# Optimization experiments

Hardware: AMD Instinct MI355X
Metric: run time of the kernel (lower is better)

Reference implementation:

```python
import jax, jax.numpy as jnp
import numpy as np

B, L, H = 32, 256, 128
VOCAB = 10


def _conv1d(h, w, b, dilation):
    # h: [B, C_in, T], w: [C_out, C_in, K] (torch OIH layout), 'same' padding = dilation for K=3
    y = jax.lax.conv_general_dilated(
        h, w, window_strides=(1,), padding=[(dilation, dilation)],
        rhs_dilation=(dilation,), dimension_numbers=("NCH", "OIH", "NCH"))
    return y + b[None, :, None]


def setup_inputs() -> dict:
    key = jax.random.key(0)
    ks = jax.random.split(key, 8)
    x = jax.random.randint(ks[0], (B, L), 0, VOCAB)
    emb_w = jax.random.normal(ks[1], (VOCAB, H), dtype=jnp.float32)
    red_w = jax.random.normal(ks[2], (H, 2 * H, 1), dtype=jnp.float32) * 0.05
    red_b = jax.random.normal(ks[3], (H,), dtype=jnp.float32) * 0.05
    conv_w = jax.random.normal(ks[4], (H, H, 3), dtype=jnp.float32) * 0.002
    conv_b = jax.random.normal(ks[5], (H,), dtype=jnp.float32) * 0.01
    out_w = jax.random.normal(ks[6], (VOCAB, H, 1), dtype=jnp.float32) * 0.1
    out_b = jax.random.normal(ks[7], (VOCAB,), dtype=jnp.float32) * 0.1
    return {"x": x, "emb_w": emb_w, "red_w": red_w, "red_b": red_b,
            "conv_w": conv_w, "conv_b": conv_b, "out_w": out_w, "out_b": out_b}


def reference(x, emb_w, red_w, red_b, conv_w, conv_b, out_w, out_b):
    digits = L // 2
    x_emb = emb_w[x].transpose(0, 2, 1)                 # [B, H, L]
    cat = jnp.concatenate([x_emb[:, :, :digits], x_emb[:, :, digits:]], axis=1)  # [B, 2H, digits]
    # reducer: 1x1 conv == pointwise matmul
    h = jax.nn.relu(jnp.einsum('oc,bct->bot', red_w[:, :, 0], cat) + red_b[None, :, None])
    h = jnp.pad(h, ((0, 0), (0, 0), (0, 1)))            # [B, H, digits+1]
    loop_count = digits + 1 + 2                          # = digits + 3
    # first 8 iterations: dilation 1 (i<4) then 2 (i<8); remainder uses dilation 4
    for i in range(min(8, loop_count)):
        d = 1 if i < 4 else 2
        h = jax.nn.relu(_conv1d(h, conv_w, conv_b, d)) + h
    def step(hc, _):
        hc = jax.nn.relu(_conv1d(hc, conv_w, conv_b, 4)) + hc
        return hc, None
    h, _ = jax.lax.scan(step, h, None, length=max(0, loop_count - 8))
    out = jnp.einsum('oc,bct->bot', out_w[:, :, 0], h) + out_b[None, :, None]  # [B, 10, digits+1]
    return out.transpose(0, 2, 1)                        # [B, digits+1, 10]
```

## Files before the change

kernel.cpp:

```cpp
#include <hip/hip_runtime.h>

typedef __attribute__((ext_vector_type(8))) short short8;
typedef __attribute__((ext_vector_type(4))) float f32x4;
typedef __attribute__((ext_vector_type(16))) float f32x16;

#define I2ROWS 40
#define I2STRIDE (I2ROWS * 128)
#define P1ROWS 72
#define P1STRIDE (P1ROWS * 128)
#define GWOFF 1056768

template<int N> struct IC { static constexpr int v = N; };

static __device__ __forceinline__ unsigned packbf(float hi, float lo) {
    return __builtin_amdgcn_perm(__float_as_uint(hi) + 0x8000u,
                                 __float_as_uint(lo) + 0x8000u, 0x07060302u);
}
static __device__ __forceinline__ unsigned short one_bf(float f) {
    return (unsigned short)((__float_as_uint(f) + 0x8000u) >> 16);
}
static __device__ __forceinline__ float bflo(unsigned u) { return __uint_as_float(u << 16); }
static __device__ __forceinline__ float bfhi(unsigned u) { return __uint_as_float(u & 0xffff0000u); }

static __device__ __forceinline__ int swzB(int row, int c) {
    return row * 128 + (c ^ ((row & 15) << 3));
}
static __device__ __forceinline__ int swzH(int t, int o) {
    return (t * 128 + o) ^ ((t & 15) << 1);
}

__global__ __launch_bounds__(256, 1)
void vgt_tab(const float* __restrict__ emb_w, const float* __restrict__ red_w,
             float* __restrict__ tab)
{
    int i = blockIdx.x * 256 + threadIdx.x;
    if (i >= 2560) return;
    int o = i / 20, col = i % 20, v = (col < 10) ? col : (col - 10);
    const float4* rw = (const float4*)(red_w + o * 256 + ((col < 10) ? 0 : 128));
    const float4* ew = (const float4*)(emb_w + v * 128);
    float s = 0.f;
#pragma unroll 8
    for (int c2 = 0; c2 < 32; ++c2) {
        float4 a = rw[c2], e = ew[c2];
        s += a.x * e.x + a.y * e.y + a.z * e.z + a.w * e.w;
    }
    tab[i] = s;
}

__global__ __launch_bounds__(256, 1)
void vgt_phase1(const int* __restrict__ x,
                const float* __restrict__ red_b,
                const float* __restrict__ conv_w,
                const float* __restrict__ conv_b,
                const float* __restrict__ tab,
                unsigned short* __restrict__ gw16)
{
    __shared__ short imgC[2 * P1STRIDE];
    __shared__ float hrFC[64 * 128];
    __shared__ float tabS[2560];
    __shared__ float cbS[128];
    __shared__ float rbS[128];
    __shared__ int   xbS[256];

    const int bid = blockIdx.x, b = bid >> 2, c = bid & 3;
    const int os = c * 33, oe = (os + 33 > 129) ? 129 : (os + 33), ws = os - 14;
    const int tid = threadIdx.x, lane = tid & 63;
    const int wm = tid >> 6, obase = wm * 32;
    const int l31 = lane & 31, lhi = lane >> 5;

    for (int i = tid; i < P1STRIDE; i += 256) ((int*)imgC)[i] = 0;
    for (int i = tid; i < 2560; i += 256) tabS[i] = tab[i];
    xbS[tid] = x[b * 256 + tid];
    if (tid < 128) { cbS[tid] = conv_b[tid]; rbS[tid] = red_b[tid]; }

    short8 aw[24];
#pragma unroll
    for (int s = 0; s < 24; ++s) {
        int kk = s >> 3, cb = s & 7;
        int o = obase + l31, c0 = cb * 16 + lhi * 8;
        short8 v;
#pragma unroll
        for (int j = 0; j < 8; ++j)
            v[j] = (short)one_bf(conv_w[(o * 128 + c0 + j) * 3 + kk]);
        aw[s] = v;
    }
    __syncthreads();

    for (int i = tid; i < 68 * 64; i += 256) {
        int rr = i >> 6, o2 = (i & 63) * 2, t = ws - 2 + rr;
        float v0 = 0.f, v1 = 0.f;
        if (t >= 0 && t < 128) {
            int x1 = xbS[t], x2 = xbS[t + 128];
            v0 = tabS[o2 * 20 + x1] + tabS[o2 * 20 + 10 + x2] + rbS[o2];
            v0 = v0 > 0.f ? v0 : 0.f;
            v1 = tabS[(o2 + 1) * 20 + x1] + tabS[(o2 + 1) * 20 + 10 + x2] + rbS[o2 + 1];
            v1 = v1 > 0.f ? v1 : 0.f;
            *(unsigned*)&imgC[swzB(rr, o2)] = packbf(v1, v0);
        }
        int rm = rr - 2;
        if (rm >= 0 && rm < 64) *(float2*)&hrFC[swzH(rm, o2)] = make_float2(v0, v1);
    }
    __syncthreads();

    int cur = 0;
    auto tileC = [&](auto DDC, int n, const short* src, short* dst) {
        constexpr int DD = decltype(DDC)::v;
        f32x16 a0, a1, a2;
#pragma unroll
        for (int g = 0; g < 4; ++g) {
            float4 bv = *(const float4*)&cbS[obase + 8 * g + 4 * lhi];
            a0[4*g+0] = bv.x; a0[4*g+1] = bv.y; a0[4*g+2] = bv.z; a0[4*g+3] = bv.w;
            a1[4*g+0] = 0.f; a1[4*g+1] = 0.f; a1[4*g+2] = 0.f; a1[4*g+3] = 0.f;
            a2[4*g+0] = 0.f; a2[4*g+1] = 0.f; a2[4*g+2] = 0.f; a2[4*g+3] = 0.f;
        }
        const int rb0 = n * 32 + l31 + 2 - DD;
#define TAPC(KK, ACC) { const int row = rb0 + KK * DD; \
    _Pragma("unroll") for (int cb = 0; cb < 8; ++cb) { \
        short8 bf = *(const short8*)&src[swzB(row, cb * 16 + lhi * 8)]; \
        ACC = __builtin_amdgcn_mfma_f32_32x32x16_bf16(aw[KK * 8 + cb], bf, ACC, 0, 0, 0); } }
        TAPC(0, a0) TAPC(1, a1) TAPC(2, a2)
#undef TAPC
        const int t = ws + n * 32 + l31;
        if (t >= 0 && t <= 128) {
            const int rm = n * 32 + l31;
#pragma unroll
            for (int g = 0; g < 4; ++g) {
                const int o4 = obase + 8 * g + 4 * lhi;
                const int h0 = swzH(rm, o4), h1 = swzH(rm, o4 + 2);
                float2 ha = *(const float2*)&hrFC[h0];
                float2 hb = *(const float2*)&hrFC[h1];
                ha.x += fmaxf(a0[4*g+0] + a1[4*g+0] + a2[4*g+0], 0.f);
                ha.y += fmaxf(a0[4*g+1] + a1[4*g+1] + a2[4*g+1], 0.f);
                hb.x += fmaxf(a0[4*g+2] + a1[4*g+2] + a2[4*g+2], 0.f);
                hb.y += fmaxf(a0[4*g+3] + a1[4*g+3] + a2[4*g+3], 0.f);
                *(float2*)&hrFC[h0] = ha;
                *(float2*)&hrFC[h1] = hb;
                *(uint2*)&dst[swzB(rm + 2, o4)] =
                    make_uint2(packbf(ha.y, ha.x), packbf(hb.y, hb.x));
            }
        }
    };
    auto step1 = [&](auto DDC) {
        const short* src = imgC + cur * P1STRIDE;
        short*       dst = imgC + (cur ^ 1) * P1STRIDE;
        tileC(DDC, 0, src, dst);
        tileC(DDC, 1, src, dst);
        __syncthreads();
        cur ^= 1;
    };
    for (int i = 0; i < 4; ++i) step1(IC<1>{});
    for (int i = 0; i < 4; ++i) step1(IC<2>{});

    for (int i = tid; i < (oe - os) * 128; i += 256) {
        int t = os + (i >> 7), o = i & 127;
        gw16[b * 16512 + t * 128 + o] = one_bf(hrFC[swzH(t - ws, o)]);
    }
}

__global__ __launch_bounds__(512, 1)
void vgt_phase2(const float* __restrict__ conv_w,
                const float* __restrict__ conv_b,
                const float* __restrict__ out_w,
                const float* __restrict__ out_b,
                const unsigned short* __restrict__ gw16,
                float* __restrict__ out)
{
    __shared__ short    img2[2 * I2STRIDE];
    __shared__ float    hrF2[33 * 128];
    __shared__ unsigned owP[10][64];
    __shared__ float    cbS[128];
    __shared__ float    obS[16];

    const int bid = blockIdx.x, b = bid >> 2, r = bid & 3;
    const int tid = threadIdx.x, lane = tid & 63;
    const int wv = tid >> 6;
    const int obase = wv * 16;
    const int l15 = lane & 15, g4 = lane >> 4;

    for (int i = tid; i < I2STRIDE; i += 512) ((int*)img2)[i] = 0;
    if (tid < 128) cbS[tid] = conv_b[tid];
    if (tid < 16)  obS[tid] = (tid < 10) ? out_b[tid] : 0.f;
    for (int i = tid; i < 640; i += 512) {
        int v = i >> 6, j = i & 63;
        owP[v][j] = packbf(out_w[v * 128 + 2 * j + 1], out_w[v * 128 + 2 * j]);
    }

    short8 aw[12];
#pragma unroll
    for (int s = 0; s < 12; ++s) {
        int kk = s >> 2, kb = s & 3;
        int o = obase + l15, c0 = kb * 32 + g4 * 8;
        short8 v;
#pragma unroll
        for (int j = 0; j < 8; ++j)
            v[j] = (short)one_bf(conv_w[(o * 128 + c0 + j) * 3 + kk]);
        aw[s] = v;
    }

    const unsigned short* gb = gw16 + b * 16512;
    float hm[2][4], hA[4];
#pragma unroll
    for (int tt = 0; tt < 2; ++tt) {
        int tp = tt * 16 + l15;
#pragma unroll
        for (int q = 0; q < 4; ++q)
            hm[tt][q] = bflo((unsigned)gb[(4 * tp + r) * 128 + obase + g4 * 4 + q]);
    }
#pragma unroll
    for (int q = 0; q < 4; ++q)
        hA[q] = (r == 0) ? bflo((unsigned)gb[16384 + obase + g4 * 4 + q]) : 0.f;

    int aM[12], aA[8], aWr, aWA;
#pragma unroll
    for (int s = 0; s < 12; ++s)
        aM[s] = 2 * swzB(l15 + (s >> 2), (s & 3) * 32 + g4 * 8);
#pragma unroll
    for (int s = 0; s < 8; ++s)
        aA[s] = 2 * swzB(32 + (s >> 2), (s & 3) * 32 + g4 * 8);
    aWr = 2 * swzB(l15 + 1, obase + g4 * 4);
    aWA = 2 * swzB(33, obase + g4 * 4);

    __syncthreads();

    float bias4[4];
#pragma unroll
    for (int q = 0; q < 4; ++q) bias4[q] = cbS[obase + g4 * 4 + q];

    for (int i = tid; i < 33 * 64; i += 512) {
        int tp = i >> 6, o2 = (i & 63) * 2;
        if (tp < 32) {
            unsigned u0 = gb[(4 * tp + r) * 128 + o2], u1 = gb[(4 * tp + r) * 128 + o2 + 1];
            *(unsigned*)&img2[swzB(tp + 1, o2)] = (u1 << 16) | u0;
        } else if (r == 0) {
            unsigned u0 = gb[16384 + o2], u1 = gb[16384 + o2 + 1];
            *(unsigned*)&img2[swzB(33, o2)] = (u1 << 16) | u0;
        }
    }
    __syncthreads();

    char* const ibase = (char*)img2;

    auto stepF = [&](auto SO_, auto DO_) {
        constexpr int SO = decltype(SO_)::v;
        constexpr int DO = decltype(DO_)::v;
        f32x4 c00, c01, c10, c11;
#pragma unroll
        for (int q = 0; q < 4; ++q) {
            c00[q] = bias4[q]; c10[q] = bias4[q];
            c01[q] = 0.f; c11[q] = 0.f;
        }
#pragma unroll
        for (int s = 0; s < 8; ++s) {
            short8 b0 = *(const short8*)(ibase + aM[s] + SO);
            short8 b1 = *(const short8*)(ibase + aM[s] + 4096 + SO);
            c00 = __builtin_amdgcn_mfma_f32_16x16x32_bf16(aw[s], b0, c00, 0, 0, 0);
            c10 = __builtin_amdgcn_mfma_f32_16x16x32_bf16(aw[s], b1, c10, 0, 0, 0);
        }
#pragma unroll
        for (int s = 8; s < 12; ++s) {
            short8 b0 = *(const short8*)(ibase + aM[s] + SO);
            short8 b1 = *(const short8*)(ibase + aM[s] + 4096 + SO);
            c01 = __builtin_amdgcn_mfma_f32_16x16x32_bf16(aw[s], b0, c01, 0, 0, 0);
            c11 = __builtin_amdgcn_mfma_f32_16x16x32_bf16(aw[s], b1, c11, 0, 0, 0);
        }
        {
#pragma unroll
            for (int q = 0; q < 4; ++q) hm[0][q] += fmaxf(c00[q] + c01[q], 0.f);
            *(uint2*)(ibase + aWr + DO) =
                make_uint2(packbf(hm[0][1], hm[0][0]), packbf(hm[0][3], hm[0][2]));
#pragma unroll
            for (int q = 0; q < 4; ++q) hm[1][q] += fmaxf(c10[q] + c11[q], 0.f);
            *(uint2*)(ibase + aWr + 4096 + DO) =
                make_uint2(packbf(hm[1][1], hm[1][0]), packbf(hm[1][3], hm[1][2]));
        }
        if (r == 0) {
            f32x4 d0, d1;
#pragma unroll
            for (int q = 0; q < 4; ++q) { d0[q] = bias4[q]; d1[q] = 0.f; }
#pragma unroll
            for (int s = 0; s < 4; ++s) {
                short8 bf = *(const short8*)(ibase + aA[s] + SO);
                d0 = __builtin_amdgcn_mfma_f32_16x16x32_bf16(aw[s], bf, d0, 0, 0, 0);
            }
#pragma unroll
            for (int s = 4; s < 8; ++s) {
                short8 bf = *(const short8*)(ibase + aA[s] + SO);
                d1 = __builtin_amdgcn_mfma_f32_16x16x32_bf16(aw[s], bf, d1, 0, 0, 0);
            }
#pragma unroll
            for (int q = 0; q < 4; ++q) hA[q] += fmaxf(d0[q] + d1[q], 0.f);
            if (l15 == 0)
                *(uint2*)(ibase + aWA + DO) =
                    make_uint2(packbf(hA[1], hA[0]), packbf(hA[3], hA[2]));
        }
        __syncthreads();
    };

    for (int i2 = 0; i2 < 61; ++i2) {
        stepF(IC<0>{}, IC<10240>{});
        stepF(IC<10240>{}, IC<0>{});
    }
    stepF(IC<0>{}, IC<10240>{});

#pragma unroll
    for (int tt = 0; tt < 2; ++tt)
        *(float4*)&hrF2[(tt * 16 + l15) * 128 + obase + g4 * 4] =
            make_float4(hm[tt][0], hm[tt][1], hm[tt][2], hm[tt][3]);
    if (r == 0 && l15 == 0)
        *(float4*)&hrF2[32 * 128 + obase + g4 * 4] =
            make_float4(hA[0], hA[1], hA[2], hA[3]);
    __syncthreads();

    const int g4h = tid & 3;
    const int tt = tid >> 2;
    const int TR = (r == 0) ? 33 : 32;
    if (tt < TR) {
        float hq[32];
#pragma unroll
        for (int j = 0; j < 8; ++j) {
            float4 v = *(const float4*)&hrF2[tt * 128 + 32 * g4h + 4 * j];
            hq[4*j+0] = v.x; hq[4*j+1] = v.y; hq[4*j+2] = v.z; hq[4*j+3] = v.w;
        }
#pragma unroll
        for (int v = 0; v < 10; ++v) {
            float s = 0.f;
#pragma unroll
            for (int i = 0; i < 16; ++i) {
                unsigned w = owP[v][16 * g4h + i];
                s += hq[2*i] * bflo(w) + hq[2*i+1] * bfhi(w);
            }
            s += __shfl_xor(s, 1);
            s += __shfl_xor(s, 2);
            if (g4h == 0) out[(b * 129 + 4 * tt + r) * 10 + v] = s + obS[v];
        }
    }
}

extern "C" void kernel_launch(void* const* d_in, const int* in_sizes, int n_in,
                              void* d_out, int out_size, void* d_ws, size_t ws_size,
                              hipStream_t stream) {
    const int*   x      = (const int*)d_in[0];
    const float* emb_w  = (const float*)d_in[1];
    const float* red_w  = (const float*)d_in[2];
    const float* red_b  = (const float*)d_in[3];
    const float* conv_w = (const float*)d_in[4];
    const float* conv_b = (const float*)d_in[5];
    const float* out_w  = (const float*)d_in[6];
    const float* out_b  = (const float*)d_in[7];
    (void)in_sizes; (void)n_in; (void)ws_size; (void)out_size;
    unsigned short* gw16 = (unsigned short*)d_ws;
    float* tab = (float*)((char*)d_ws + GWOFF);
    vgt_tab<<<10, 256, 0, stream>>>(emb_w, red_w, tab);
    vgt_phase1<<<128, 256, 0, stream>>>(x, red_b, conv_w, conv_b, tab, gw16);
    vgt_phase2<<<128, 512, 0, stream>>>(conv_w, conv_b, out_w, out_b, gw16, (float*)d_out);
}
```

Measured before the change: 170.4 us.

## Split conv reduction across wave pairs with LDS partial-sum exchange

Changes the phase-2 work split so each wave computes a 32-output by 64-channel tile, with two wave roles that each cover half the input channels. Partial sums go through a new LDS buffer and are combined by the role-0 waves, which own the residual state. Each B-operand load from the image now feeds four MFMAs instead of two, cutting LDS reads per MFMA. In exchange every step gains an extra barrier plus LDS write/read traffic for the partials, and the serial 123-step recurrence is latency bound.

```diff
diff --git a/kernel.cpp b/kernel.cpp
--- a/kernel.cpp
+++ b/kernel.cpp
@@ -166,6 +166,7 @@
                 float* __restrict__ out)
 {
     __shared__ short    img2[2 * I2STRIDE];
+    __shared__ float    pbuf[6 * 1024];
     __shared__ float    hrF2[33 * 128];
     __shared__ unsigned owP[10][64];
     __shared__ float    cbS[128];
@@ -174,7 +175,10 @@
     const int bid = blockIdx.x, b = bid >> 2, r = bid & 3;
     const int tid = threadIdx.x, lane = tid & 63;
     const int wv = tid >> 6;
-    const int obase = wv * 16;
+    const int pr = wv & 3;
+    const int role = wv >> 2;
+    const int obase = pr * 32;
+    const int chbase = role * 64;
     const int l15 = lane & 15, g4 = lane >> 4;
 
     for (int i = tid; i < I2STRIDE; i += 512) ((int*)img2)[i] = 0;
@@ -187,44 +191,63 @@
 
     short8 aw[12];
 #pragma unroll
-    for (int s = 0; s < 12; ++s) {
-        int kk = s >> 2, kb = s & 3;
-        int o = obase + l15, c0 = kb * 32 + g4 * 8;
-        short8 v;
-#pragma unroll
-        for (int j = 0; j < 8; ++j)
-            v[j] = (short)one_bf(conv_w[(o * 128 + c0 + j) * 3 + kk]);
-        aw[s] = v;
+    for (int s = 0; s < 6; ++s) {
+        int kk = s >> 1, cb = s & 1;
+        int c0 = chbase + cb * 32 + g4 * 8;
+#pragma unroll
+        for (int mt = 0; mt < 2; ++mt) {
+            int o = obase + mt * 16 + l15;
+            short8 v;
+#pragma unroll
+            for (int j = 0; j < 8; ++j)
+                v[j] = (short)one_bf(conv_w[(o * 128 + c0 + j) * 3 + kk]);
+            aw[s * 2 + mt] = v;
+        }
     }
 
     const unsigned short* gb = gw16 + b * 16512;
-    float hm[2][4], hA[4];
-#pragma unroll
-    for (int tt = 0; tt < 2; ++tt) {
-        int tp = tt * 16 + l15;
-#pragma unroll
-        for (int q = 0; q < 4; ++q)
-            hm[tt][q] = bflo((unsigned)gb[(4 * tp + r) * 128 + obase + g4 * 4 + q]);
-    }
-#pragma unroll
-    for (int q = 0; q < 4; ++q)
-        hA[q] = (r == 0) ? bflo((unsigned)gb[16384 + obase + g4 * 4 + q]) : 0.f;
-
-    int aM[12], aA[8], aWr, aWA;
-#pragma unroll
-    for (int s = 0; s < 12; ++s)
-        aM[s] = 2 * swzB(l15 + (s >> 2), (s & 3) * 32 + g4 * 8);
-#pragma unroll
-    for (int s = 0; s < 8; ++s)
-        aA[s] = 2 * swzB(32 + (s >> 2), (s & 3) * 32 + g4 * 8);
-    aWr = 2 * swzB(l15 + 1, obase + g4 * 4);
-    aWA = 2 * swzB(33, obase + g4 * 4);
+
+    float hm00[4], hm01[4], hm10[4], hm11[4];
+    float hA0[4], hA1[4];
+    if (role == 0) {
+#pragma unroll
+        for (int q = 0; q < 4; ++q) {
+            hm00[q] = bflo((unsigned)gb[(4 * l15 + r) * 128 + obase + g4 * 4 + q]);
+            hm01[q] = bflo((unsigned)gb[(4 * l15 + r) * 128 + obase + 16 + g4 * 4 + q]);
+            hm10[q] = bflo((unsigned)gb[(4 * (16 + l15) + r) * 128 + obase + g4 * 4 + q]);
+            hm11[q] = bflo((unsigned)gb[(4 * (16 + l15) + r) * 128 + obase + 16 + g4 * 4 + q]);
+        }
+    } else {
+#pragma unroll
+        for (int q = 0; q < 4; ++q) {
+            hA0[q] = (r == 0) ? bflo((unsigned)gb[16384 + obase + g4 * 4 + q]) : 0.f;
+            hA1[q] = (r == 0) ? bflo((unsigned)gb[16384 + obase + 16 + g4 * 4 + q]) : 0.f;
+        }
+    }
+
+    int aM[6], aA[4], aW00, aW01, aW10, aW11, aWA0, aWA1;
+#pragma unroll
+    for (int s = 0; s < 6; ++s)
+        aM[s] = 2 * swzB(l15 + (s >> 1), chbase + (s & 1) * 32 + g4 * 8);
+#pragma unroll
+    for (int s = 0; s < 4; ++s)
+        aA[s] = 2 * swzB(32 + (s >> 1), chbase + (s & 1) * 32 + g4 * 8);
+    aW00 = 2 * swzB(l15 + 1, obase + g4 * 4);
+    aW01 = 2 * swzB(l15 + 1, obase + 16 + g4 * 4);
+    aW10 = 2 * swzB(16 + l15 + 1, obase + g4 * 4);
+    aW11 = 2 * swzB(16 + l15 + 1, obase + 16 + g4 * 4);
+    aWA0 = 2 * swzB(33, obase + g4 * 4);
+    aWA1 = 2 * swzB(33, obase + 16 + g4 * 4);
+    const int pAddr = pr * 1024 + lane * 16;
 
     __syncthreads();
 
-    float bias4[4];
-#pragma unroll
-    for (int q = 0; q < 4; ++q) bias4[q] = cbS[obase + g4 * 4 + q];
+    float bb[8];
+#pragma unroll
+    for (int q = 0; q < 4; ++q) {
+        bb[q]     = cbS[obase + g4 * 4 + q];
+        bb[4 + q] = cbS[obase + 16 + g4 * 4 + q];
+    }
 
     for (int i = tid; i < 33 * 64; i += 512) {
         int tp = i >> 6, o2 = (i & 63) * 2;
@@ -239,59 +262,87 @@
     __syncthreads();
 
     char* const ibase = (char*)img2;
+    char* const pB = (char*)pbuf;
 
     auto stepF = [&](auto SO_, auto DO_) {
         constexpr int SO = decltype(SO_)::v;
         constexpr int DO = decltype(DO_)::v;
-        f32x4 c00, c01, c10, c11;
-#pragma unroll
-        for (int q = 0; q < 4; ++q) {
-            c00[q] = bias4[q]; c10[q] = bias4[q];
-            c01[q] = 0.f; c11[q] = 0.f;
-        }
-#pragma unroll
-        for (int s = 0; s < 8; ++s) {
+        f32x4 a00, a01, a10, a11;
+#pragma unroll
+        for (int q = 0; q < 4; ++q) { a00[q] = 0.f; a01[q] = 0.f; a10[q] = 0.f; a11[q] = 0.f; }
+#pragma unroll
+        for (int s = 0; s < 6; ++s) {
             short8 b0 = *(const short8*)(ibase + aM[s] + SO);
             short8 b1 = *(const short8*)(ibase + aM[s] + 4096 + SO);
-            c00 = __builtin_amdgcn_mfma_f32_16x16x32_bf16(aw[s], b0, c00, 0, 0, 0);
-            c10 = __builtin_amdgcn_mfma_f32_16x16x32_bf16(aw[s], b1, c10, 0, 0, 0);
-        }
-#pragma unroll
-        for (int s = 8; s < 12; ++s) {
-            short8 b0 = *(const short8*)(ibase + aM[s] + SO);
-            short8 b1 = *(const short8*)(ibase + aM[s] + 4096 + SO);
-            c01 = __builtin_amdgcn_mfma_f32_16x16x32_bf16(aw[s], b0, c01, 0, 0, 0);
-            c11 = __builtin_amdgcn_mfma_f32_16x16x32_bf16(aw[s], b1, c11, 0, 0, 0);
-        }
-        {
-#pragma unroll
-            for (int q = 0; q < 4; ++q) hm[0][q] += fmaxf(c00[q] + c01[q], 0.f);
-            *(uint2*)(ibase + aWr + DO) =
-                make_uint2(packbf(hm[0][1], hm[0][0]), packbf(hm[0][3], hm[0][2]));
-#pragma unroll
-            for (int q = 0; q < 4; ++q) hm[1][q] += fmaxf(c10[q] + c11[q], 0.f);
-            *(uint2*)(ibase + aWr + 4096 + DO) =
-                make_uint2(packbf(hm[1][1], hm[1][0]), packbf(hm[1][3], hm[1][2]));
-        }
-        if (r == 0) {
-            f32x4 d0, d1;
-#pragma unroll
-            for (int q = 0; q < 4; ++q) { d0[q] = bias4[q]; d1[q] = 0.f; }
+            a00 = __builtin_amdgcn_mfma_f32_16x16x32_bf16(aw[s * 2 + 0], b0, a00, 0, 0, 0);
+            a01 = __builtin_amdgcn_mfma_f32_16x16x32_bf16(aw[s * 2 + 1], b0, a01, 0, 0, 0);
+            a10 = __builtin_amdgcn_mfma_f32_16x16x32_bf16(aw[s * 2 + 0], b1, a10, 0, 0, 0);
+            a11 = __builtin_amdgcn_mfma_f32_16x16x32_bf16(aw[s * 2 + 1], b1, a11, 0, 0, 0);
+        }
+        f32x4 ap0, ap1;
+        if (role == 1) {
+            *(f32x4*)(pB + pAddr)         = a00;
+            *(f32x4*)(pB + pAddr + 4096)  = a01;
+            *(f32x4*)(pB + pAddr + 8192)  = a10;
+            *(f32x4*)(pB + pAddr + 12288) = a11;
+            if (r == 0) {
+#pragma unroll
+                for (int q = 0; q < 4; ++q) { ap0[q] = 0.f; ap1[q] = 0.f; }
+#pragma unroll
+                for (int s = 0; s < 4; ++s) {
+                    short8 bf = *(const short8*)(ibase + aA[s] + SO);
+                    ap0 = __builtin_amdgcn_mfma_f32_16x16x32_bf16(aw[s * 2 + 0], bf, ap0, 0, 0, 0);
+                    ap1 = __builtin_amdgcn_mfma_f32_16x16x32_bf16(aw[s * 2 + 1], bf, ap1, 0, 0, 0);
+                }
+            }
+        } else if (r == 0) {
+#pragma unroll
+            for (int q = 0; q < 4; ++q) { ap0[q] = 0.f; ap1[q] = 0.f; }
 #pragma unroll
             for (int s = 0; s < 4; ++s) {
                 short8 bf = *(const short8*)(ibase + aA[s] + SO);
-                d0 = __builtin_amdgcn_mfma_f32_16x16x32_bf16(aw[s], bf, d0, 0, 0, 0);
+                ap0 = __builtin_amdgcn_mfma_f32_16x16x32_bf16(aw[s * 2 + 0], bf, ap0, 0, 0, 0);
+                ap1 = __builtin_amdgcn_mfma_f32_16x16x32_bf16(aw[s * 2 + 1], bf, ap1, 0, 0, 0);
             }
-#pragma unroll
-            for (int s = 4; s < 8; ++s) {
-                short8 bf = *(const short8*)(ibase + aA[s] + SO);
-                d1 = __builtin_amdgcn_mfma_f32_16x16x32_bf16(aw[s], bf, d1, 0, 0, 0);
+            *(f32x4*)(pB + pAddr + 16384) = ap0;
+            *(f32x4*)(pB + pAddr + 20480) = ap1;
+        }
+        __syncthreads();
+
+        if (role == 0) {
+            f32x4 p00 = *(const f32x4*)(pB + pAddr);
+            f32x4 p01 = *(const f32x4*)(pB + pAddr + 4096);
+            f32x4 p10 = *(const f32x4*)(pB + pAddr + 8192);
+            f32x4 p11 = *(const f32x4*)(pB + pAddr + 12288);
+#pragma unroll
+            for (int q = 0; q < 4; ++q) hm00[q] += fmaxf(a00[q] + p00[q] + bb[q], 0.f);
+            *(uint2*)(ibase + aW00 + DO) =
+                make_uint2(packbf(hm00[1], hm00[0]), packbf(hm00[3], hm00[2]));
+#pragma unroll
+            for (int q = 0; q < 4; ++q) hm01[q] += fmaxf(a01[q] + p01[q] + bb[4 + q], 0.f);
+            *(uint2*)(ibase + aW01 + DO) =
+                make_uint2(packbf(hm01[1], hm01[0]), packbf(hm01[3], hm01[2]));
+#pragma unroll
+            for (int q = 0; q < 4; ++q) hm10[q] += fmaxf(a10[q] + p10[q] + bb[q], 0.f);
+            *(uint2*)(ibase + aW10 + DO) =
+                make_uint2(packbf(hm10[1], hm10[0]), packbf(hm10[3], hm10[2]));
+#pragma unroll
+            for (int q = 0; q < 4; ++q) hm11[q] += fmaxf(a11[q] + p11[q] + bb[4 + q], 0.f);
+            *(uint2*)(ibase + aW11 + DO) =
+                make_uint2(packbf(hm11[1], hm11[0]), packbf(hm11[3], hm11[2]));
+        } else if (r == 0) {
+            f32x4 q0 = *(const f32x4*)(pB + pAddr + 16384);
+            f32x4 q1 = *(const f32x4*)(pB + pAddr + 20480);
+#pragma unroll
+            for (int q = 0; q < 4; ++q) hA0[q] += fmaxf(ap0[q] + q0[q] + bb[q], 0.f);
+#pragma unroll
+            for (int q = 0; q < 4; ++q) hA1[q] += fmaxf(ap1[q] + q1[q] + bb[4 + q], 0.f);
+            if (l15 == 0) {
+                *(uint2*)(ibase + aWA0 + DO) =
+                    make_uint2(packbf(hA0[1], hA0[0]), packbf(hA0[3], hA0[2]));
+                *(uint2*)(ibase + aWA1 + DO) =
+                    make_uint2(packbf(hA1[1], hA1[0]), packbf(hA1[3], hA1[2]));
             }
-#pragma unroll
-            for (int q = 0; q < 4; ++q) hA[q] += fmaxf(d0[q] + d1[q], 0.f);
-            if (l15 == 0)
-                *(uint2*)(ibase + aWA + DO) =
-                    make_uint2(packbf(hA[1], hA[0]), packbf(hA[3], hA[2]));
         }
         __syncthreads();
     };
@@ -302,13 +353,21 @@
     }
     stepF(IC<0>{}, IC<10240>{});
 
-#pragma unroll
-    for (int tt = 0; tt < 2; ++tt)
-        *(float4*)&hrF2[(tt * 16 + l15) * 128 + obase + g4 * 4] =
-            make_float4(hm[tt][0], hm[tt][1], hm[tt][2], hm[tt][3]);
-    if (r == 0 && l15 == 0)
+    if (role == 0) {
+        *(float4*)&hrF2[l15 * 128 + obase + g4 * 4] =
+            make_float4(hm00[0], hm00[1], hm00[2], hm00[3]);
+        *(float4*)&hrF2[l15 * 128 + obase + 16 + g4 * 4] =
+            make_float4(hm01[0], hm01[1], hm01[2], hm01[3]);
+        *(float4*)&hrF2[(16 + l15) * 128 + obase + g4 * 4] =
+            make_float4(hm10[0], hm10[1], hm10[2], hm10[3]);
+        *(float4*)&hrF2[(16 + l15) * 128 + obase + 16 + g4 * 4] =
+            make_float4(hm11[0], hm11[1], hm11[2], hm11[3]);
+    } else if (r == 0 && l15 == 0) {
         *(float4*)&hrF2[32 * 128 + obase + g4 * 4] =
-            make_float4(hA[0], hA[1], hA[2], hA[3]);
+            make_float4(hA0[0], hA0[1], hA0[2], hA0[3]);
+        *(float4*)&hrF2[32 * 128 + obase + 16 + g4 * 4] =
+            make_float4(hA1[0], hA1[1], hA1[2], hA1[3]);
+    }
     __syncthreads();
 
     const int g4h = tid & 3;
```

Result: slower. 183.0 us (+7.4%).
